# Kernel optimization log

Hardware: AMD Instinct MI355X
Metric: run time of the kernel (lower is better)

The kernel has to match this reference:

```python
import jax, jax.numpy as jnp
import numpy as np

B, DIM, IN_DIM, H, W = 4, 256, 128, 128, 128
DD = IN_DIM // 2          # down_dim = 64
HEADS = 8
BN_EPS = 1e-5


def conv2d(x, w, b=None, pad=0, dil=1):
    y = jax.lax.conv_general_dilated(
        x, w, window_strides=(1, 1),
        padding=[(pad, pad), (pad, pad)],
        rhs_dilation=(dil, dil),
        dimension_numbers=('NCHW', 'OIHW', 'NCHW'))
    if b is not None:
        y = y + b[None, :, None, None]
    return y


def bn_relu(x, s, o):
    # eval-mode BatchNorm2d with running_mean=0, running_var=1
    return jax.nn.relu(x * (s / np.sqrt(1.0 + BN_EPS))[None, :, None, None] + o[None, :, None, None])


def setup_inputs() -> dict:
    ks = iter(jax.random.split(jax.random.key(0), 80))

    def w(shape, sc=0.05):
        return sc * jax.random.normal(next(ks), shape, jnp.float32)

    def s(c):
        return 1.0 + 0.1 * jax.random.normal(next(ks), (c,), jnp.float32)

    def o(c):
        return 0.02 * jax.random.normal(next(ks), (c,), jnp.float32)

    d = {}
    d['x'] = jax.random.normal(next(ks), (B, DIM, H, W), jnp.float32)
    d['w_dc'] = w((IN_DIM, DIM, 3, 3)); d['b_dc'] = w((IN_DIM,)); d['s_dc'] = s(IN_DIM); d['o_dc'] = o(IN_DIM)
    d['w1'] = w((DD, IN_DIM, 1, 1)); d['b1'] = w((DD,)); d['s1'] = s(DD); d['o1'] = o(DD)
    d['w2'] = w((DD, DD, 3, 3)); d['b2'] = w((DD,)); d['s2'] = s(DD); d['o2'] = o(DD)
    d['w3'] = w((DD, DD, 3, 3)); d['b3'] = w((DD,)); d['s3'] = s(DD); d['o3'] = o(DD)
    d['w4'] = w((DD, DD, 3, 3)); d['b4'] = w((DD,)); d['s4'] = s(DD); d['o4'] = o(DD)
    d['w5'] = w((DD, IN_DIM, 1, 1)); d['b5'] = w((DD,)); d['s5'] = s(DD); d['o5'] = o(DD)
    d['temperature'] = jnp.ones((HEADS, 1, 1), jnp.float32)
    d['w_po'] = w((DD, 2 * DD, 1, 1))  # project_out, bias=False
    d['w_wa'] = w((DD // 16, DD, 1, 1)); d['b_wa'] = w((DD // 16,)); d['s_wa'] = s(DD // 16); d['o_wa'] = o(DD // 16)
    d['w_wb'] = w((DD, DD // 16, 1, 1)); d['b_wb'] = w((DD,))
    d['w_f'] = w((DD, 5 * DD, 1, 1)); d['b_f'] = w((DD,)); d['s_f'] = s(DD); d['o_f'] = o(DD)
    d['w_oa'] = w((DD // 2, DD, 3, 3)); d['b_oa'] = w((DD // 2,)); d['s_oa'] = s(DD // 2); d['o_oa'] = o(DD // 2)
    d['w_ob'] = w((1, DD // 2, 1, 1)); d['b_ob'] = w((1,))
    return d


def reference(x, w_dc, b_dc, s_dc, o_dc, w1, b1, s1, o1, w2, b2, s2, o2,
              w3, b3, s3, o3, w4, b4, s4, o4, w5, b5, s5, o5,
              temperature, w_po, w_wa, b_wa, s_wa, o_wa, w_wb, b_wb,
              w_f, b_f, s_f, o_f, w_oa, b_oa, s_oa, o_oa, w_ob, b_ob):

    def branch(c):
        b, ch, h, wd = c.shape
        f = jnp.fft.fft2(c)                                   # [b,ch,h,w] complex64 (q=k=v=tepqkv)
        qkv = f.reshape(b, HEADS, ch // HEADS, h * wd)        # v (unnormalized)
        n = jnp.sqrt(jnp.sum(jnp.square(jnp.abs(qkv)), axis=-1, keepdims=True))
        qn = qkv / jnp.maximum(n, 1e-12)                      # F.normalize(dim=-1); q == k
        attn = jnp.einsum('bhcn,bhdn->bhcd', qn, qn) * temperature
        # custom complex normalization: separate real/imag softmax
        attn = jax.lax.complex(jax.nn.softmax(attn.real, axis=-1),
                               jax.nn.softmax(attn.imag, axis=-1))
        of = jnp.abs(jnp.fft.ifft2(jnp.einsum('bhcd,bhdn->bhcn', attn, qkv)))  # ifft2 over (c, hw)
        of = of.reshape(b, ch, h, wd)
        g = jax.nn.sigmoid(conv2d(bn_relu(conv2d(f.real, w_wa, b_wa), s_wa, o_wa), w_wb, b_wb))
        ol = jnp.abs(jnp.fft.ifft2(g * f))                    # ifft2 over (h, w)
        return conv2d(jnp.concatenate([of, ol], axis=1), w_po) + c

    xd = bn_relu(conv2d(x, w_dc, b_dc, pad=1), s_dc, o_dc)
    c1 = bn_relu(conv2d(xd, w1, b1), s1, o1)
    c2 = bn_relu(conv2d(c1, w2, b2, pad=3, dil=3), s2, o2)
    F2 = branch(c2)
    c3 = bn_relu(conv2d(c1 + F2, w3, b3, pad=5, dil=5), s3, o3)
    F3 = branch(c3)
    c4 = bn_relu(conv2d(c1 + F3, w4, b4, pad=7, dil=7), s4, o4)
    F4 = branch(c4)
    # conv5: global avg pool -> 1x1 conv -> bilinear upsample of a 1x1 map == broadcast
    c5 = bn_relu(conv2d(jnp.mean(xd, axis=(2, 3), keepdims=True), w5, b5), s5, o5)
    c5 = jnp.broadcast_to(c5, (c5.shape[0], c5.shape[1], xd.shape[2], xd.shape[3]))
    fused = bn_relu(conv2d(jnp.concatenate([c1, F2, F3, F4, c5], axis=1), w_f, b_f), s_f, o_f)
    return conv2d(bn_relu(conv2d(fused, w_oa, b_oa, pad=1), s_oa, o_oa), w_ob, b_ob)
```

## Files before the change

### kernel.cpp

```cpp
#include <hip/hip_runtime.h>

#define S 16384
#define PI_F 3.14159265358979f

struct Ptrs { const float* p[43]; };

enum : int {
  O_SBDC=0, O_SB1=256, O_SB2=512, O_SB3=768, O_SB4=1024, O_SB5=1280,
  O_SBWA=1536, O_SBF=1792, O_SBOA=2048,
  O_M=2304, O_C5=2816, O_NRM=3072, O_GRAM=3328, O_ATT2=7424, O_BEFF=11520,
  O_WB=16384,
  O_PART=147456,
  O_H=180224,
  O_WP=442368,
  O_A=524288,
  O_FIN=8912896,
  O_CC=25690112,
  O_DRE=29884416, O_DIMG=34078720,
  O_ERE=38273024, O_EIM=42467328,
  O_G=46661632
};

typedef short bfrag __attribute__((ext_vector_type(8)));
typedef float ffrag __attribute__((ext_vector_type(4)));

__device__ __forceinline__ float bf2f(unsigned short u){
  union { unsigned int i; float f; } v; v.i = ((unsigned int)u) << 16; return v.f;
}
__device__ __forceinline__ unsigned short f2bf(float f){
  unsigned int x = __float_as_uint(f);
  unsigned int r = x + 0x7fffu + ((x >> 16) & 1u);
  return (unsigned short)(r >> 16);
}

__global__ void prep_sb_kernel(Ptrs P, float* ws){
  const float r = rsqrtf(1.0f + 1e-5f);
  int bi=0, si=0, oi=0, C=0, dst=0;
  switch (blockIdx.x){
    case 0: bi=2; si=3; oi=4; C=128; dst=O_SBDC; break;
    case 1: bi=6; si=7; oi=8; C=64; dst=O_SB1; break;
    case 2: bi=10; si=11; oi=12; C=64; dst=O_SB2; break;
    case 3: bi=14; si=15; oi=16; C=64; dst=O_SB3; break;
    case 4: bi=18; si=19; oi=20; C=64; dst=O_SB4; break;
    case 5: bi=22; si=23; oi=24; C=64; dst=O_SB5; break;
    case 6: bi=28; si=29; oi=30; C=4;  dst=O_SBWA; break;
    case 7: bi=34; si=35; oi=36; C=64; dst=O_SBF; break;
    default: bi=38; si=39; oi=40; C=32; dst=O_SBOA; break;
  }
  for (int c = threadIdx.x; c < C; c += 256){
    float bb = P.p[bi][c], ss = P.p[si][c], oo = P.p[oi][c];
    float sc = ss * r;
    ws[dst + c] = sc;
    ws[dst + C + c] = bb * sc + oo;
  }
}

__global__ __launch_bounds__(256) void xpad_kernel(const float* __restrict__ x,
    unsigned short* __restrict__ XT){
  int yy = blockIdx.x, b = blockIdx.y;
  long obase = ((long)(b*130) + yy) * (130L*256);
  int tid = threadIdx.x;
  if (yy == 0 || yy == 129){
    uint4 z; z.x=0; z.y=0; z.z=0; z.w=0;
    for (int i = tid; i < 130*256/8; i += 256)
      *(uint4*)(XT + obase + (long)i*8) = z;
    return;
  }
  __shared__ float LT[64][129];
  int y = yy - 1;
  for (int c0 = 0; c0 < 256; c0 += 64){
    for (int idx = tid; idx < 64*128; idx += 256){
      int ci = idx >> 7, xx = idx & 127;
      LT[ci][xx] = x[((long)(b*256 + c0 + ci)*128 + y)*128 + xx];
    }
    __syncthreads();
    for (int idx = tid; idx < 128*16; idx += 256){
      int xp = idx >> 4, c4 = (idx & 15)*4;
      ushort4 v;
      v.x = f2bf(LT[c4][xp]);   v.y = f2bf(LT[c4+1][xp]);
      v.z = f2bf(LT[c4+2][xp]); v.w = f2bf(LT[c4+3][xp]);
      *(ushort4*)(XT + obase + (long)(xp+1)*256 + c0 + c4) = v;
    }
    __syncthreads();
  }
  if (tid < 64){
    ushort4 z; z.x=0; z.y=0; z.z=0; z.w=0;
    *(ushort4*)(XT + obase + tid*4) = z;
    *(ushort4*)(XT + obase + 129L*256 + tid*4) = z;
  }
}

__global__ void wt_kernel(const float* __restrict__ w, unsigned short* __restrict__ WH,
    unsigned short* __restrict__ WL){
  for (int e = blockIdx.x*256 + threadIdx.x; e < 294912; e += gridDim.x*256){
    int c32 = e & 31, co = (e >> 5) & 127, kc = (e >> 12) & 7, sh = e >> 15;
    int ky = sh / 3, kx = sh - ky*3;
    int ci = kc*32 + c32;
    float v = w[((long)(co*256 + ci)*3 + ky)*3 + kx];
    unsigned short h = f2bf(v);
    WH[e] = h;
    WL[e] = f2bf(v - bf2f(h));
  }
}

__global__ void wtg_kernel(Ptrs P, unsigned short* __restrict__ WB){
  const float* w; int cout; long off;
  switch (blockIdx.y){
    case 0: w = P.p[9];  cout = 64; off = 0;      break;
    case 1: w = P.p[13]; cout = 64; off = 73728;  break;
    case 2: w = P.p[17]; cout = 64; off = 147456; break;
    default: w = P.p[37]; cout = 32; off = 221184; break;
  }
  int total = 576*cout;
  unsigned short* WH = WB + off;
  unsigned short* WL = WH + total;
  for (int e = blockIdx.x*256 + threadIdx.x; e < total; e += gridDim.x*256){
    int c32 = e & 31;
    int co = (e >> 5) & (cout - 1);
    int kc = (e / (32*cout)) & 1;
    int sh = e / (64*cout);
    int ky = sh/3, kx = sh - ky*3;
    int ci = kc*32 + c32;
    float v = w[((long)(co*64 + ci)*3 + ky)*3 + kx];
    unsigned short h = f2bf(v);
    WH[e] = h;
    WL[e] = f2bf(v - bf2f(h));
  }
}

__global__ void wtp_kernel(Ptrs P, unsigned short* __restrict__ WP){
  const float* w; int KC, wstr; long off;
  switch (blockIdx.y){
    case 0: w = P.p[5];  KC = 4; wstr = 128; off = 0;     break;
    case 1: w = P.p[26]; KC = 4; wstr = 128; off = 16384; break;
    default: w = P.p[33]; KC = 8; wstr = 320; off = 32768; break;
  }
  int total = KC*64*32;
  unsigned short* WH = WP + off;
  unsigned short* WL = WH + total;
  for (int e = blockIdx.x*256 + threadIdx.x; e < total; e += gridDim.x*256){
    int c32 = e & 31, co = (e >> 5) & 63, kc = e >> 11;
    float v = w[(long)co*wstr + kc*32 + c32];
    unsigned short h = f2bf(v);
    WH[e] = h;
    WL[e] = f2bf(v - bf2f(h));
  }
}

template<int DIL>
__global__ __launch_bounds__(256) void xpad64_kernel(const float* __restrict__ in1,
    const float* __restrict__ in2, long in_bs, unsigned short* __restrict__ XP){
  constexpr int TW = 128 + 2*DIL;
  int yy = blockIdx.x, b = blockIdx.y;
  long obase = (long)(b*TW + yy) * TW * 64;
  int tid = threadIdx.x;
  if (yy < DIL || yy >= 128 + DIL){
    uint4 z; z.x=0; z.y=0; z.z=0; z.w=0;
    for (int i = tid; i < TW*8; i += 256)
      *(uint4*)(XP + obase + (long)i*8) = z;
    return;
  }
  __shared__ float LT[64][129];
  int y = yy - DIL;
  const float* p1 = in1 + (long)b*in_bs + (long)y*128;
  const float* p2 = in2 ? in2 + (long)b*in_bs + (long)y*128 : nullptr;
  for (int idx = tid; idx < 64*128; idx += 256){
    int ci = idx >> 7, xx = idx & 127;
    float v = p1[(long)ci*S + xx];
    if (p2) v += p2[(long)ci*S + xx];
    LT[ci][xx] = v;
  }
  __syncthreads();
  for (int i = tid; i < 2*DIL*16; i += 256){
    int side = i / (DIL*16);
    int r = i - side*(DIL*16);
    int xcol = side ? (128 + DIL + (r >> 4)) : (r >> 4);
    ushort4 z; z.x=0; z.y=0; z.z=0; z.w=0;
    *(ushort4*)(XP + obase + (long)xcol*64 + (r & 15)*4) = z;
  }
  for (int idx = tid; idx < 128*16; idx += 256){
    int xp = idx >> 4, c4 = (idx & 15)*4;
    ushort4 v;
    v.x = f2bf(LT[c4][xp]);   v.y = f2bf(LT[c4+1][xp]);
    v.z = f2bf(LT[c4+2][xp]); v.w = f2bf(LT[c4+3][xp]);
    *(ushort4*)(XP + obase + (long)(xp + DIL)*64 + c4) = v;
  }
}

template<int DIL, int KC, int NBLK>
__global__ __launch_bounds__(256) void conv3x3_mfma_kernel(
    const unsigned short* __restrict__ XP,
    const unsigned short* __restrict__ WH, const unsigned short* __restrict__ WL,
    const float* __restrict__ scbi, float* __restrict__ out){
  constexpr int CIN = KC*32;
  constexpr int TW = 128 + 2*DIL;
  constexpr int STEPS = 9*KC;
  constexpr int MI = (NBLK == 64) ? 4 : 2;
  constexpr int LDA = 36;
  __shared__ unsigned short Als[128*LDA];
  __shared__ unsigned short BHs[NBLK*LDA];
  __shared__ unsigned short BLs[NBLK*LDA];
  int bid = blockIdx.x;
  int y = (bid & 7)*16 + ((bid >> 3) & 15);
  int b = (bid >> 7) & 3;
  int n2 = bid >> 9;
  int nb = gridDim.x >> 9; if (nb == 0) nb = 1;
  int coutTotal = nb * NBLK;
  int tid = threadIdx.x, wv = tid >> 6, lane = tid & 63;
  int mt0 = (NBLK == 64) ? (wv & 1)*4 : wv*2;
  int nt0 = (NBLK == 64) ? (wv >> 1)*2 : 0;
  ffrag acc[MI][2];
  #pragma unroll
  for (int i = 0; i < MI; i++)
    #pragma unroll
    for (int j = 0; j < 2; j++)
      #pragma unroll
      for (int r = 0; r < 4; r++) acc[i][j][r] = 0.f;

  int pixq = tid >> 2, qq = tid & 3;
  int kq = (lane >> 4)*8, rown = lane & 15;
  int wrA0 = pixq*LDA + qq*8;
  int wrA1 = (pixq + 64)*LDA + qq*8;
  int wrB  = (tid >> 2)*LDA + qq*8;

  uint4 A0, A1, BHr, BLr;
  {
    long abase = ((long)(b*TW + y)*TW)*CIN + qq*8;
    A0 = *(const uint4*)(XP + abase + (long)pixq*CIN);
    A1 = *(const uint4*)(XP + abase + (long)(pixq + 64)*CIN);
    long gw = (long)n2*NBLK*32;
    if (NBLK == 64 || tid < 128){
      BHr = *(const uint4*)(WH + gw + tid*8);
      BLr = *(const uint4*)(WL + gw + tid*8);
    }
  }
  for (int step = 0; step < STEPS; step++){
    __syncthreads();
    *(uint4*)&Als[wrA0] = A0;
    *(uint4*)&Als[wrA1] = A1;
    if (NBLK == 64 || tid < 128){
      *(uint4*)&BHs[wrB] = BHr;
      *(uint4*)&BLs[wrB] = BLr;
    }
    __syncthreads();
    if (step + 1 < STEPS){
      int s2 = step + 1;
      int sh = s2 / KC, kc = s2 - sh*KC;
      int ky = sh / 3, kx = sh - ky*3;
      long abase = ((long)(b*TW + y + ky*DIL)*TW + kx*DIL)*CIN + kc*32 + qq*8;
      A0 = *(const uint4*)(XP + abase + (long)pixq*CIN);
      A1 = *(const uint4*)(XP + abase + (long)(pixq + 64)*CIN);
      long gw = ((long)s2*coutTotal + n2*NBLK)*32;
      if (NBLK == 64 || tid < 128){
        BHr = *(const uint4*)(WH + gw + tid*8);
        BLr = *(const uint4*)(WL + gw + tid*8);
      }
    }
    bfrag af[MI], bhf[2], blf[2];
    #pragma unroll
    for (int i = 0; i < MI; i++)
      af[i] = *(const bfrag*)&Als[((mt0 + i)*16 + rown)*LDA + kq];
    #pragma unroll
    for (int j = 0; j < 2; j++){
      bhf[j] = *(const bfrag*)&BHs[((nt0 + j)*16 + rown)*LDA + kq];
      blf[j] = *(const bfrag*)&BLs[((nt0 + j)*16 + rown)*LDA + kq];
    }
    #pragma unroll
    for (int i = 0; i < MI; i++)
      #pragma unroll
      for (int j = 0; j < 2; j++){
        acc[i][j] = __builtin_amdgcn_mfma_f32_16x16x32_bf16(af[i], blf[j], acc[i][j], 0, 0, 0);
        acc[i][j] = __builtin_amdgcn_mfma_f32_16x16x32_bf16(af[i], bhf[j], acc[i][j], 0, 0, 0);
      }
  }
  #pragma unroll
  for (int i = 0; i < MI; i++){
    int pixel = (mt0 + i)*16 + (lane >> 4)*4;
    #pragma unroll
    for (int j = 0; j < 2; j++){
      int co = n2*NBLK + (nt0 + j)*16 + (lane & 15);
      float sc = scbi[co], bb = scbi[coutTotal + co];
      float* op = out + ((long)(b*coutTotal + co))*S + y*128 + pixel;
      #pragma unroll
      for (int r = 0; r < 4; r++)
        op[r] = fmaxf(acc[i][j][r]*sc + bb, 0.f);
    }
  }
}

template<int MODE, int KC, int BF16IN>
__global__ __launch_bounds__(256) void conv1x1_mfma_kernel(
    const void* __restrict__ inv, long in_bs,
    const unsigned short* __restrict__ WH, const unsigned short* __restrict__ WL,
    const float* __restrict__ scbi, const float* __restrict__ beff,
    const float* __restrict__ res, long res_bs,
    float* __restrict__ out, long out_bs){
  constexpr int LDA = 36;
  __shared__ unsigned short Als[128*LDA];
  __shared__ unsigned short BHs[64*LDA];
  __shared__ unsigned short BLs[64*LDA];
  int bid = blockIdx.x;
  int y = (bid & 7)*16 + ((bid >> 3) & 15);
  int b = bid >> 7;
  int tid = threadIdx.x, wv = tid >> 6, lane = tid & 63;
  int mt0 = (wv & 1)*4, nt0 = (wv >> 1)*2;
  ffrag acc[4][2];
  #pragma unroll
  for (int i = 0; i < 4; i++)
    #pragma unroll
    for (int j = 0; j < 2; j++)
      #pragma unroll
      for (int r = 0; r < 4; r++) acc[i][j][r] = 0.f;
  int pq = tid & 31, cg = tid >> 5;
  int kq = (lane >> 4)*8, rown = lane & 15;
  int wrB = (tid >> 2)*LDA + (tid & 3)*8;
  const float* ibf = (const float*)inv + (long)b*in_bs + y*128;
  const unsigned short* ibs = (const unsigned short*)inv + (long)b*in_bs + y*128;
  unsigned short a[16];
  uint4 BHr, BLr;
  #pragma unroll
  for (int cc = 0; cc < 4; cc++)
    #pragma unroll
    for (int i = 0; i < 4; i++){
      if (BF16IN) a[cc*4 + i] = ibs[(long)(cg*4 + cc)*S + pq + 32*i];
      else        a[cc*4 + i] = f2bf(ibf[(long)(cg*4 + cc)*S + pq + 32*i]);
    }
  BHr = *(const uint4*)(WH + tid*8);
  BLr = *(const uint4*)(WL + tid*8);
  for (int kc = 0; kc < KC; kc++){
    __syncthreads();
    #pragma unroll
    for (int i = 0; i < 4; i++){
      ushort4 v;
      v.x = a[0 + i];  v.y = a[4 + i];
      v.z = a[8 + i];  v.w = a[12 + i];
      *(ushort4*)&Als[(pq + 32*i)*LDA + cg*4] = v;
    }
    *(uint4*)&BHs[wrB] = BHr;
    *(uint4*)&BLs[wrB] = BLr;
    __syncthreads();
    if (kc + 1 < KC){
      #pragma unroll
      for (int cc = 0; cc < 4; cc++)
        #pragma unroll
        for (int i = 0; i < 4; i++){
          long off = (long)((kc + 1)*32 + cg*4 + cc)*S + pq + 32*i;
          if (BF16IN) a[cc*4 + i] = ibs[off];
          else        a[cc*4 + i] = f2bf(ibf[off]);
        }
      long gw = (long)(kc + 1)*2048;
      BHr = *(const uint4*)(WH + gw + tid*8);
      BLr = *(const uint4*)(WL + gw + tid*8);
    }
    bfrag af[4], bhf[2], blf[2];
    #pragma unroll
    for (int i = 0; i < 4; i++)
      af[i] = *(const bfrag*)&Als[((mt0 + i)*16 + rown)*LDA + kq];
    #pragma unroll
    for (int j = 0; j < 2; j++){
      bhf[j] = *(const bfrag*)&BHs[((nt0 + j)*16 + rown)*LDA + kq];
      blf[j] = *(const bfrag*)&BLs[((nt0 + j)*16 + rown)*LDA + kq];
    }
    #pragma unroll
    for (int i = 0; i < 4; i++)
      #pragma unroll
      for (int j = 0; j < 2; j++){
        acc[i][j] = __builtin_amdgcn_mfma_f32_16x16x32_bf16(af[i], blf[j], acc[i][j], 0, 0, 0);
        acc[i][j] = __builtin_amdgcn_mfma_f32_16x16x32_bf16(af[i], bhf[j], acc[i][j], 0, 0, 0);
      }
  }
  #pragma unroll
  for (int i = 0; i < 4; i++){
    int pixel = (mt0 + i)*16 + (lane >> 4)*4;
    #pragma unroll
    for (int j = 0; j < 2; j++){
      int co = (nt0 + j)*16 + (lane & 15);
      float* op = out + (long)b*out_bs + (long)co*S + y*128 + pixel;
      #pragma unroll
      for (int r = 0; r < 4; r++){
        float v = acc[i][j][r];
        if (MODE == 0){
          v = fmaxf(v*scbi[co] + scbi[64 + co], 0.f);
        } else if (MODE == 1){
          v += res[(long)b*res_bs + (long)co*S + y*128 + pixel + r];
        } else {
          v = fmaxf(v*scbi[co] + beff[b*64 + co], 0.f);
        }
        op[r] = v;
      }
    }
  }
}

__device__ __forceinline__ void fft128_mk_tw(float (&tws)[8], float (&twc)[8],
                                             float sign, int lane){
  float a0 = sign * (2.0f*PI_F/128.0f) * (float)lane;
  __sincosf(a0, &tws[0], &twc[0]);
  int i = 1;
  #pragma unroll
  for (int h = 32; h >= 1; h >>= 1, i++){
    int j = lane & (h - 1);
    float a = sign * (2.0f*PI_F/128.0f) * (float)(j * (64/h));
    __sincosf(a, &tws[i], &twc[i]);
  }
}

__device__ __forceinline__ void fft128(float& z0r, float& z0i, float& z1r, float& z1i,
    const float (&tws)[8], const float (&twc)[8], int lane){
  {
    float ar = z0r, ai = z0i, br = z1r, bi = z1i;
    z0r = ar + br; z0i = ai + bi;
    float dr = ar - br, di = ai - bi;
    float s = tws[0], c = twc[0];
    z1r = dr*c - di*s; z1i = dr*s + di*c;
  }
  int idx = 1;
  #pragma unroll
  for (int h = 32; h >= 1; h >>= 1, idx++){
    float s = tws[idx], c = twc[idx];
    bool up = (lane & h) != 0;
    float pr, pi, nr, ni;
    pr = __shfl_xor(z0r, h, 64); pi = __shfl_xor(z0i, h, 64);
    if (!up){ nr = z0r + pr; ni = z0i + pi; }
    else { float dr = pr - z0r, di = pi - z0i; nr = dr*c - di*s; ni = dr*s + di*c; }
    z0r = nr; z0i = ni;
    pr = __shfl_xor(z1r, h, 64); pi = __shfl_xor(z1i, h, 64);
    if (!up){ nr = z1r + pr; ni = z1i + pi; }
    else { float dr = pr - z1r, di = pi - z1i; nr = dr*c - di*s; ni = dr*s + di*c; }
    z1r = nr; z1i = ni;
  }
}

__global__ __launch_bounds__(256) void fft_rows_fwd_kernel(const float* __restrict__ in,
    unsigned short* __restrict__ outRe, unsigned short* __restrict__ outIm){
  int line = blockIdx.x*4 + (threadIdx.x >> 6);
  int lane = threadIdx.x & 63;
  float tws[8], twc[8];
  fft128_mk_tw(tws, twc, -1.0f, lane);
  long ib = (long)line * 128;
  float z0r = in[ib + lane], z0i = 0.f;
  float z1r = in[ib + lane + 64], z1i = 0.f;
  fft128(z0r, z0i, z1r, z1i, tws, twc, lane);
  int k = __brev(lane) >> 25;
  ushort2 vr; vr.x = f2bf(z0r); vr.y = f2bf(z1r);
  ushort2 vi; vi.x = f2bf(z0i); vi.y = f2bf(z1i);
  *(ushort2*)(outRe + ib + k) = vr;
  *(ushort2*)(outIm + ib + k) = vi;
}

template<int MODE>
__global__ __launch_bounds__(256) void fft_cols_kernel(
    const unsigned short* inRe, const unsigned short* inIm,
    unsigned short* outRe, unsigned short* outIm,
    const float* gate, const float* wb, const float* bwb){
  __shared__ float lre[128][17];
  __shared__ float lim[128][17];
  int plane = blockIdx.y;
  int cb = blockIdx.x * 16;
  int tid = threadIdx.x;
  long pbase = (long)plane * S;
  float w0=0.f, w1=0.f, w2=0.f, w3=0.f, bw=0.f;
  const float* Hb = nullptr;
  if (MODE == 1){
    int co = plane & 63;
    w0 = wb[co*4]; w1 = wb[co*4+1]; w2 = wb[co*4+2]; w3 = wb[co*4+3];
    bw = bwb[co];
    Hb = gate + (long)(plane >> 6) * 4 * S;
  }
  #pragma unroll
  for (int i = 0; i < 8; i++){
    int idx = tid + i*256;
    int r = idx >> 4, c = idx & 15;
    int pxl = r*128 + cb + c;
    long a = pbase + pxl;
    float re = bf2f(inRe[a]), im = bf2f(inIm[a]);
    if (MODE == 1){
      float hv = bw + w0*Hb[pxl] + w1*Hb[S + pxl] + w2*Hb[2*S + pxl] + w3*Hb[3*S + pxl];
      float g = 1.0f / (1.0f + __expf(-hv));
      re *= g; im *= g;
    }
    lre[r][c] = re; lim[r][c] = im;
  }
  __syncthreads();
  int wv = tid >> 6, lane = tid & 63;
  const float sign = (MODE == 0) ? -1.0f : 1.0f;
  float tws[8], twc[8];
  fft128_mk_tw(tws, twc, sign, lane);
  #pragma unroll
  for (int cc = 0; cc < 4; cc++){
    int c = wv*4 + cc;
    float z0r = lre[lane][c], z0i = lim[lane][c];
    float z1r = lre[lane + 64][c], z1i = lim[lane + 64][c];
    fft128(z0r, z0i, z1r, z1i, tws, twc, lane);
    int k = __brev(lane) >> 25;
    if (MODE == 2){
      int n2 = cb + c;
      float s, co;
      float a0 = (2.0f*PI_F/16384.0f) * (float)(n2 * k);
      __sincosf(a0, &s, &co);
      float t = z0r*co - z0i*s; z0i = z0r*s + z0i*co; z0r = t;
      float a1 = (2.0f*PI_F/16384.0f) * (float)(n2 * (k + 1));
      __sincosf(a1, &s, &co);
      t = z1r*co - z1i*s; z1i = z1r*s + z1i*co; z1r = t;
    }
    lre[k][c] = z0r;     lim[k][c] = z0i;
    lre[k + 1][c] = z1r; lim[k + 1][c] = z1i;
  }
  __syncthreads();
  #pragma unroll
  for (int i = 0; i < 8; i++){
    int idx = tid + i*256;
    int r = idx >> 4, c = idx & 15;
    long a = pbase + r*128 + cb + c;
    outRe[a] = f2bf(lre[r][c]); outIm[a] = f2bf(lim[r][c]);
  }
}

__global__ __launch_bounds__(256) void ifft_rows_abs_ol_kernel(
    const unsigned short* __restrict__ Ere, const unsigned short* __restrict__ Eim,
    unsigned short* __restrict__ AB){
  int line = blockIdx.x*4 + (threadIdx.x >> 6);
  int lane = threadIdx.x & 63;
  float tws[8], twc[8];
  fft128_mk_tw(tws, twc, 1.0f, lane);
  int plane = line >> 7, row = line & 127;
  long ib = (long)plane*S + row*128;
  float z0r = bf2f(Ere[ib + lane]), z0i = bf2f(Eim[ib + lane]);
  float z1r = bf2f(Ere[ib + lane + 64]), z1i = bf2f(Eim[ib + lane + 64]);
  fft128(z0r, z0i, z1r, z1i, tws, twc, lane);
  int b = plane >> 6, ch = plane & 63;
  unsigned short* out = AB + ((long)(b*128 + 64 + ch)) * S + row*128;
  int k = __brev(lane) >> 25;
  ushort2 v;
  v.x = f2bf(sqrtf(z0r*z0r + z0i*z0i) * (1.0f/16384.0f));
  v.y = f2bf(sqrtf(z1r*z1r + z1i*z1i) * (1.0f/16384.0f));
  *(ushort2*)(out + k) = v;
}

__global__ __launch_bounds__(256) void ifft_rows_abs_ofT_kernel(
    const unsigned short* __restrict__ Ere, const unsigned short* __restrict__ Eim,
    unsigned short* __restrict__ AB){
  __shared__ float T[128][17];
  int plane = blockIdx.y;
  int r0 = blockIdx.x * 16;
  int wv = threadIdx.x >> 6, lane = threadIdx.x & 63;
  float tws[8], twc[8];
  fft128_mk_tw(tws, twc, 1.0f, lane);
  #pragma unroll
  for (int i = 0; i < 4; i++){
    int rl = wv*4 + i;
    int row = r0 + rl;
    long ib = (long)plane*S + row*128;
    float z0r = bf2f(Ere[ib + lane]), z0i = bf2f(Eim[ib + lane]);
    float z1r = bf2f(Ere[ib + lane + 64]), z1i = bf2f(Eim[ib + lane + 64]);
    fft128(z0r, z0i, z1r, z1i, tws, twc, lane);
    int k = __brev(lane) >> 25;
    T[k][rl]     = sqrtf(z0r*z0r + z0i*z0i) * (1.0f/16384.0f);
    T[k + 1][rl] = sqrtf(z1r*z1r + z1i*z1i) * (1.0f/16384.0f);
  }
  __syncthreads();
  int b = plane >> 6, ch = plane & 63;
  unsigned short* out = AB + ((long)(b*128 + ch)) * S + r0;
  #pragma unroll
  for (int i = 0; i < 8; i++){
    int idx = threadIdx.x + i*256;
    int k2 = idx >> 4, rl = idx & 15;
    out[(long)k2*128 + rl] = f2bf(T[k2][rl]);
  }
}

__global__ __launch_bounds__(256) void gram_part_kernel(
    const unsigned short* __restrict__ Dre, const unsigned short* __restrict__ Dim,
    float* __restrict__ PART){
  int bh = blockIdx.x, slab = blockIdx.y;
  long base = (long)bh * 8 * S;
  int n0 = slab * 2048;
  float accr[36], acci[36], nsq[8];
  #pragma unroll
  for (int i = 0; i < 36; i++){ accr[i] = 0.f; acci[i] = 0.f; }
  #pragma unroll
  for (int i = 0; i < 8; i++) nsq[i] = 0.f;
  for (int it = 0; it < 8; it++){
    int n = n0 + it*256 + threadIdx.x;
    float xr[8], xi[8];
    #pragma unroll
    for (int c = 0; c < 8; c++){
      xr[c] = bf2f(Dre[base + (long)c*S + n]);
      xi[c] = bf2f(Dim[base + (long)c*S + n]);
      nsq[c] += xr[c]*xr[c] + xi[c]*xi[c];
    }
    int t = 0;
    #pragma unroll
    for (int c = 0; c < 8; c++)
      #pragma unroll
      for (int d = c; d < 8; d++){
        accr[t] += xr[c]*xr[d] - xi[c]*xi[d];
        acci[t] += xr[c]*xi[d] + xi[c]*xr[d];
        t++;
      }
  }
  __shared__ float red[4][80];
  int wv = threadIdx.x >> 6, lane = threadIdx.x & 63;
  #pragma unroll
  for (int i = 0; i < 80; i++){
    float v = (i < 36) ? accr[i] : (i < 72) ? acci[i - 36] : nsq[i - 72];
    #pragma unroll
    for (int o = 32; o; o >>= 1) v += __shfl_xor(v, o, 64);
    if (lane == 0) red[wv][i] = v;
  }
  __syncthreads();
  if (threadIdx.x < 80){
    int i = threadIdx.x;
    PART[(long)(bh*8 + slab)*80 + i] = red[0][i] + red[1][i] + red[2][i] + red[3][i];
  }
}

__global__ void attn2f_kernel(const float* __restrict__ PART,
    const float* __restrict__ temp, float* __restrict__ ATT2){
  __shared__ float ssum[80];
  __shared__ float sar[64], sai[64];
  int bh = blockIdx.x;
  int t = threadIdx.x;
  if (t < 80){
    float s = 0.f;
    for (int i = 0; i < 8; i++) s += PART[(long)(bh*8 + i)*80 + t];
    ssum[t] = s;
  }
  __syncthreads();
  if (t >= 64) return;
  int lane = t;
  int c = lane >> 3, d = lane & 7;
  int lo = min(c, d), hi = max(c, d);
  int t2 = lo*8 - lo*(lo - 1)/2 + (hi - lo);
  float nnc = fmaxf(sqrtf(ssum[72 + c]), 1e-12f);
  float nnd = fmaxf(sqrtf(ssum[72 + d]), 1e-12f);
  float inv = temp[bh & 7] / (nnc * nnd);
  float ar = ssum[t2] * inv, ai = ssum[36 + t2] * inv;
  float m = ar;
  m = fmaxf(m, __shfl_xor(m, 1, 64)); m = fmaxf(m, __shfl_xor(m, 2, 64)); m = fmaxf(m, __shfl_xor(m, 4, 64));
  float e = __expf(ar - m);
  float su = e;
  su += __shfl_xor(su, 1, 64); su += __shfl_xor(su, 2, 64); su += __shfl_xor(su, 4, 64);
  ar = e / su;
  m = ai;
  m = fmaxf(m, __shfl_xor(m, 1, 64)); m = fmaxf(m, __shfl_xor(m, 2, 64)); m = fmaxf(m, __shfl_xor(m, 4, 64));
  e = __expf(ai - m);
  su = e;
  su += __shfl_xor(su, 1, 64); su += __shfl_xor(su, 2, 64); su += __shfl_xor(su, 4, 64);
  ai = e / su;
  sar[lane] = ar; sai[lane] = ai;
  __syncthreads();
  const float ct[8] = {1.f, 0.70710678f, 0.f, -0.70710678f, -1.f, -0.70710678f, 0.f, 0.70710678f};
  const float st[8] = {0.f, 0.70710678f, 1.f, 0.70710678f, 0.f, -0.70710678f, -1.f, -0.70710678f};
  int cp = c;
  float sr = 0.f, si = 0.f;
  #pragma unroll
  for (int cc = 0; cc < 8; cc++){
    int k = (cc * cp) & 7;
    float a = sar[cc*8 + d], b2 = sai[cc*8 + d];
    sr += ct[k]*a - st[k]*b2;
    si += ct[k]*b2 + st[k]*a;
  }
  float2 v; v.x = sr * 0.125f; v.y = si * 0.125f;
  ((float2*)ATT2)[bh*64 + lane] = v;
}

__global__ __launch_bounds__(256) void apply_attn_kernel(
    const unsigned short* __restrict__ Dre, const unsigned short* __restrict__ Dim,
    const float* __restrict__ ATT2,
    unsigned short* __restrict__ Ere, unsigned short* __restrict__ Eim){
  int bh = blockIdx.y;
  int px = blockIdx.x*1024 + (threadIdx.x & 63)*4 + (threadIdx.x >> 6)*256;
  long base = (long)bh * 8 * S + px;
  float4 ar[8], ai[8];
  #pragma unroll
  for (int i = 0; i < 8; i++){
    ar[i].x = ar[i].y = ar[i].z = ar[i].w = 0.f;
    ai[i].x = ai[i].y = ai[i].z = ai[i].w = 0.f;
  }
  #pragma unroll
  for (int d = 0; d < 8; d++){
    ushort4 ur = *(const ushort4*)(Dre + base + (long)d*S);
    ushort4 ui = *(const ushort4*)(Dim + base + (long)d*S);
    float4 xr, xi;
    xr.x = bf2f(ur.x); xr.y = bf2f(ur.y); xr.z = bf2f(ur.z); xr.w = bf2f(ur.w);
    xi.x = bf2f(ui.x); xi.y = bf2f(ui.y); xi.z = bf2f(ui.z); xi.w = bf2f(ui.w);
    #pragma unroll
    for (int cp = 0; cp < 8; cp++){
      float wr = ATT2[bh*128 + (cp*8 + d)*2];
      float wi = ATT2[bh*128 + (cp*8 + d)*2 + 1];
      ar[cp].x += wr*xr.x - wi*xi.x;  ai[cp].x += wr*xi.x + wi*xr.x;
      ar[cp].y += wr*xr.y - wi*xi.y;  ai[cp].y += wr*xi.y + wi*xr.y;
      ar[cp].z += wr*xr.z - wi*xi.z;  ai[cp].z += wr*xi.z + wi*xr.z;
      ar[cp].w += wr*xr.w - wi*xi.w;  ai[cp].w += wr*xi.w + wi*xr.w;
    }
  }
  #pragma unroll
  for (int cp = 0; cp < 8; cp++){
    ushort4 vr, vi;
    vr.x = f2bf(ar[cp].x); vr.y = f2bf(ar[cp].y); vr.z = f2bf(ar[cp].z); vr.w = f2bf(ar[cp].w);
    vi.x = f2bf(ai[cp].x); vi.y = f2bf(ai[cp].y); vi.z = f2bf(ai[cp].z); vi.w = f2bf(ai[cp].w);
    *(ushort4*)(Ere + base + (long)cp*S) = vr;
    *(ushort4*)(Eim + base + (long)cp*S) = vi;
  }
}

__global__ __launch_bounds__(256) void gateh_kernel(const unsigned short* __restrict__ Dre,
    const float* __restrict__ wa, const float* __restrict__ sbwa, float* __restrict__ H){
  int b = blockIdx.y;
  int px = blockIdx.x*256 + threadIdx.x;
  long base = (long)b * 64 * S + px;
  float h0 = 0.f, h1 = 0.f, h2 = 0.f, h3 = 0.f;
  for (int ci = 0; ci < 64; ci++){
    float x = bf2f(Dre[base + (long)ci*S]);
    h0 += wa[ci]*x; h1 += wa[64 + ci]*x; h2 += wa[128 + ci]*x; h3 += wa[192 + ci]*x;
  }
  long ob = (long)b * 4 * S + px;
  H[ob]       = fmaxf(h0*sbwa[0] + sbwa[4], 0.f);
  H[ob + S]   = fmaxf(h1*sbwa[1] + sbwa[5], 0.f);
  H[ob + 2*S] = fmaxf(h2*sbwa[2] + sbwa[6], 0.f);
  H[ob + 3*S] = fmaxf(h3*sbwa[3] + sbwa[7], 0.f);
}

__global__ __launch_bounds__(256) void mean_kernel(const float* __restrict__ A, float* __restrict__ M){
  int p = blockIdx.x;
  long base = (long)p * S;
  float s = 0.f;
  for (int n = threadIdx.x; n < S; n += 256) s += A[base + n];
  #pragma unroll
  for (int o = 32; o; o >>= 1) s += __shfl_xor(s, o, 64);
  __shared__ float sm[4];
  if ((threadIdx.x & 63) == 0) sm[threadIdx.x >> 6] = s;
  __syncthreads();
  if (threadIdx.x == 0) M[p] = (sm[0] + sm[1] + sm[2] + sm[3]) * (1.0f/16384.0f);
}

__global__ void c5_kernel(const float* __restrict__ W5, const float* __restrict__ sb5,
    const float* __restrict__ M, float* __restrict__ C5){
  int t = threadIdx.x;
  if (t >= 256) return;
  int b = t >> 6, co = t & 63;
  float s = 0.f;
  for (int ci = 0; ci < 128; ci++) s += W5[co*128 + ci] * M[b*128 + ci];
  C5[t] = fmaxf(s * sb5[co] + sb5[64 + co], 0.f);
}

__global__ void beff_kernel(const float* __restrict__ WF, const float* __restrict__ sbf,
    const float* __restrict__ C5, float* __restrict__ BEFF){
  int t = threadIdx.x;
  if (t >= 256) return;
  int b = t >> 6, co = t & 63;
  float s = 0.f;
  for (int j = 0; j < 64; j++) s += WF[co*320 + 256 + j] * C5[b*64 + j];
  BEFF[t] = s * sbf[co] + sbf[64 + co];
}

__global__ __launch_bounds__(256) void ob_kernel(const float* __restrict__ Tin,
    const float* __restrict__ wob, const float* __restrict__ bob, float* __restrict__ out){
  int b = blockIdx.y;
  int px = blockIdx.x*1024 + (threadIdx.x & 63)*4 + (threadIdx.x >> 6)*256;
  float b0 = bob[0];
  float4 a; a.x = b0; a.y = b0; a.z = b0; a.w = b0;
  for (int ci = 0; ci < 32; ci++){
    float4 v = *(const float4*)(Tin + ((long)b*32 + ci)*S + px);
    float w = wob[ci];
    a.x += w*v.x; a.y += w*v.y; a.z += w*v.z; a.w += w*v.w;
  }
  *(float4*)(out + (long)b*S + px) = a;
}

extern "C" void kernel_launch(void* const* d_in, const int* in_sizes, int n_in,
                              void* d_out, int out_size, void* d_ws, size_t ws_size,
                              hipStream_t stream){
  float* ws = (float*)d_ws;
  Ptrs P;
  for (int i = 0; i < 43 && i < n_in; i++) P.p[i] = (const float*)d_in[i];
  float* out = (float*)d_out;

  float* A   = ws + O_A;
  float* FIN = ws + O_FIN;
  float* CC  = ws + O_CC;
  float* G   = ws + O_G;
  float* H   = ws + O_H;

  unsigned short* DRE16 = (unsigned short*)(ws + O_DRE);
  unsigned short* DIM16 = (unsigned short*)(ws + O_DIMG);
  unsigned short* ERE16 = (unsigned short*)(ws + O_ERE);
  unsigned short* EIM16 = (unsigned short*)(ws + O_EIM);
  unsigned short* AB    = (unsigned short*)(ws + O_A);

  unsigned short* XT  = (unsigned short*)(ws + O_DRE);
  unsigned short* WHd = (unsigned short*)(ws + O_CC);
  unsigned short* WLd = (unsigned short*)(ws + O_CC + 147456);
  unsigned short* WB  = (unsigned short*)(ws + O_WB);
  unsigned short* WP  = (unsigned short*)(ws + O_WP);
  unsigned short* XP  = (unsigned short*)(ws + O_ERE);

  prep_sb_kernel<<<dim3(9), dim3(256), 0, stream>>>(P, ws);
  xpad_kernel<<<dim3(130, 4), dim3(256), 0, stream>>>(P.p[0], XT);
  wt_kernel<<<dim3(128), dim3(256), 0, stream>>>(P.p[1], WHd, WLd);
  wtg_kernel<<<dim3(16, 4), dim3(256), 0, stream>>>(P, WB);
  wtp_kernel<<<dim3(8, 3), dim3(256), 0, stream>>>(P, WP);

  conv3x3_mfma_kernel<1,8,64><<<dim3(1024), dim3(256), 0, stream>>>(
      XT, WHd, WLd, ws + O_SBDC, A);

  mean_kernel<<<dim3(512), dim3(256), 0, stream>>>(A, ws + O_M);
  c5_kernel<<<dim3(1), dim3(256), 0, stream>>>(P.p[21], ws + O_SB5, ws + O_M, ws + O_C5);
  beff_kernel<<<dim3(1), dim3(256), 0, stream>>>(P.p[33], ws + O_SBF, ws + O_C5, ws + O_BEFF);

  conv1x1_mfma_kernel<0,4,0><<<dim3(512), dim3(256), 0, stream>>>(
      A, 128*S, WP, WP + 8192, ws + O_SB1, nullptr, nullptr, 0, FIN, 256*S);

  for (int k = 0; k < 3; k++){
    const float* sb = ws + (k == 0 ? O_SB2 : k == 1 ? O_SB3 : O_SB4);
    const float* in2 = (k == 0) ? nullptr : FIN + (long)(64*k)*S;
    unsigned short* wh = WB + (k == 0 ? 0 : k == 1 ? 73728 : 147456);
    if (k == 0){
      xpad64_kernel<3><<<dim3(134, 4), dim3(256), 0, stream>>>(FIN, in2, 256*S, XP);
      conv3x3_mfma_kernel<3,2,64><<<dim3(512), dim3(256), 0, stream>>>(
          XP, wh, wh + 36864, sb, CC);
    } else if (k == 1){
      xpad64_kernel<5><<<dim3(138, 4), dim3(256), 0, stream>>>(FIN, in2, 256*S, XP);
      conv3x3_mfma_kernel<5,2,64><<<dim3(512), dim3(256), 0, stream>>>(
          XP, wh, wh + 36864, sb, CC);
    } else {
      xpad64_kernel<7><<<dim3(142, 4), dim3(256), 0, stream>>>(FIN, in2, 256*S, XP);
      conv3x3_mfma_kernel<7,2,64><<<dim3(512), dim3(256), 0, stream>>>(
          XP, wh, wh + 36864, sb, CC);
    }

    fft_rows_fwd_kernel<<<dim3(8192), dim3(256), 0, stream>>>(CC, DRE16, DIM16);
    fft_cols_kernel<0><<<dim3(8, 256), dim3(256), 0, stream>>>(
        DRE16, DIM16, DRE16, DIM16, nullptr, nullptr, nullptr);
    gram_part_kernel<<<dim3(32, 8), dim3(256), 0, stream>>>(DRE16, DIM16, ws + O_PART);
    attn2f_kernel<<<dim3(32), dim3(128), 0, stream>>>(ws + O_PART, P.p[25], ws + O_ATT2);
    gateh_kernel<<<dim3(64, 4), dim3(256), 0, stream>>>(DRE16, P.p[27], ws + O_SBWA, H);
    fft_cols_kernel<1><<<dim3(8, 256), dim3(256), 0, stream>>>(
        DRE16, DIM16, ERE16, EIM16, H, P.p[31], P.p[32]);
    ifft_rows_abs_ol_kernel<<<dim3(8192), dim3(256), 0, stream>>>(ERE16, EIM16, AB);
    apply_attn_kernel<<<dim3(16, 32), dim3(256), 0, stream>>>(DRE16, DIM16, ws + O_ATT2, ERE16, EIM16);
    fft_cols_kernel<2><<<dim3(8, 256), dim3(256), 0, stream>>>(
        ERE16, EIM16, ERE16, EIM16, nullptr, nullptr, nullptr);
    ifft_rows_abs_ofT_kernel<<<dim3(8, 256), dim3(256), 0, stream>>>(ERE16, EIM16, AB);
    conv1x1_mfma_kernel<1,4,1><<<dim3(512), dim3(256), 0, stream>>>(
        AB, 128*S, WP + 16384, WP + 24576, nullptr, nullptr, CC, 64*S,
        FIN + (long)(64*(k + 1))*S, 256*S);
  }

  conv1x1_mfma_kernel<2,8,0><<<dim3(512), dim3(256), 0, stream>>>(
      FIN, 256*S, WP + 32768, WP + 49152, ws + O_SBF, ws + O_BEFF, nullptr, 0, CC, 64*S);
  xpad64_kernel<1><<<dim3(130, 4), dim3(256), 0, stream>>>(CC, nullptr, 64*S, XP);
  conv3x3_mfma_kernel<1,2,32><<<dim3(512), dim3(256), 0, stream>>>(
      XP, WB + 221184, WB + 221184 + 18432, ws + O_SBOA, G);
  ob_kernel<<<dim3(16, 4), dim3(256), 0, stream>>>(G, P.p[41], P.p[42], out);
}
```

Before: 984.2 us.

## Fuse row and column FFT passes into whole-plane 2D FFT kernels in LDS

Replaces the separate row-FFT and column-FFT kernels (three pairs per branch) with single kernels that each hold a whole 128x128 complex plane in shared memory and do both passes with 1024 threads per block. This drops the bf16 intermediate round trips through global memory and cuts the number of launches. The cost is about 132KB of LDS per block, so only one block fits per CU, and each grid has just 256 blocks, which lowers occupancy and latency hiding. It also keeps intermediates in fp32 rather than bf16 between the two passes.

After: 909.4 us. 1.08x faster.

```diff
diff --git a/kernel.cpp b/kernel.cpp
--- a/kernel.cpp
+++ b/kernel.cpp
@@ -431,141 +431,163 @@
   }
 }
 
-__global__ __launch_bounds__(256) void fft_rows_fwd_kernel(const float* __restrict__ in,
+
+__global__ __launch_bounds__(1024) void fft2_fwd_kernel(const float* __restrict__ in,
     unsigned short* __restrict__ outRe, unsigned short* __restrict__ outIm){
-  int line = blockIdx.x*4 + (threadIdx.x >> 6);
-  int lane = threadIdx.x & 63;
+  __shared__ float lre[128][129];
+  __shared__ float lim[128][129];
+  int plane = blockIdx.x;
+  int tid = threadIdx.x, wv = tid >> 6, lane = tid & 63;
+  long pbase = (long)plane * S;
+  for (int i = tid; i < S/4; i += 1024){
+    int px = i*4; int r = px >> 7, c = px & 127;
+    float4 v = *(const float4*)(in + pbase + px);
+    lre[r][c] = v.x; lre[r][c+1] = v.y; lre[r][c+2] = v.z; lre[r][c+3] = v.w;
+  }
   float tws[8], twc[8];
   fft128_mk_tw(tws, twc, -1.0f, lane);
-  long ib = (long)line * 128;
-  float z0r = in[ib + lane], z0i = 0.f;
-  float z1r = in[ib + lane + 64], z1i = 0.f;
-  fft128(z0r, z0i, z1r, z1i, tws, twc, lane);
-  int k = __brev(lane) >> 25;
-  ushort2 vr; vr.x = f2bf(z0r); vr.y = f2bf(z1r);
-  ushort2 vi; vi.x = f2bf(z0i); vi.y = f2bf(z1i);
-  *(ushort2*)(outRe + ib + k) = vr;
-  *(ushort2*)(outIm + ib + k) = vi;
-}
-
-template<int MODE>
-__global__ __launch_bounds__(256) void fft_cols_kernel(
-    const unsigned short* inRe, const unsigned short* inIm,
-    unsigned short* outRe, unsigned short* outIm,
-    const float* gate, const float* wb, const float* bwb){
-  __shared__ float lre[128][17];
-  __shared__ float lim[128][17];
-  int plane = blockIdx.y;
-  int cb = blockIdx.x * 16;
-  int tid = threadIdx.x;
-  long pbase = (long)plane * S;
-  float w0=0.f, w1=0.f, w2=0.f, w3=0.f, bw=0.f;
-  const float* Hb = nullptr;
-  if (MODE == 1){
-    int co = plane & 63;
-    w0 = wb[co*4]; w1 = wb[co*4+1]; w2 = wb[co*4+2]; w3 = wb[co*4+3];
-    bw = bwb[co];
-    Hb = gate + (long)(plane >> 6) * 4 * S;
-  }
-  #pragma unroll
-  for (int i = 0; i < 8; i++){
-    int idx = tid + i*256;
-    int r = idx >> 4, c = idx & 15;
-    int pxl = r*128 + cb + c;
-    long a = pbase + pxl;
-    float re = bf2f(inRe[a]), im = bf2f(inIm[a]);
-    if (MODE == 1){
-      float hv = bw + w0*Hb[pxl] + w1*Hb[S + pxl] + w2*Hb[2*S + pxl] + w3*Hb[3*S + pxl];
-      float g = 1.0f / (1.0f + __expf(-hv));
-      re *= g; im *= g;
-    }
-    lre[r][c] = re; lim[r][c] = im;
-  }
-  __syncthreads();
-  int wv = tid >> 6, lane = tid & 63;
-  const float sign = (MODE == 0) ? -1.0f : 1.0f;
-  float tws[8], twc[8];
-  fft128_mk_tw(tws, twc, sign, lane);
-  #pragma unroll
-  for (int cc = 0; cc < 4; cc++){
-    int c = wv*4 + cc;
+  __syncthreads();
+  #pragma unroll
+  for (int rr = 0; rr < 8; rr++){
+    int r = wv*8 + rr;
+    float z0r = lre[r][lane], z0i = 0.f;
+    float z1r = lre[r][lane + 64], z1i = 0.f;
+    fft128(z0r, z0i, z1r, z1i, tws, twc, lane);
+    int k = __brev(lane) >> 25;
+    lre[r][k] = z0r;     lim[r][k] = z0i;
+    lre[r][k+1] = z1r;   lim[r][k+1] = z1i;
+  }
+  __syncthreads();
+  #pragma unroll
+  for (int cc = 0; cc < 8; cc++){
+    int c = wv*8 + cc;
     float z0r = lre[lane][c], z0i = lim[lane][c];
     float z1r = lre[lane + 64][c], z1i = lim[lane + 64][c];
     fft128(z0r, z0i, z1r, z1i, tws, twc, lane);
     int k = __brev(lane) >> 25;
-    if (MODE == 2){
-      int n2 = cb + c;
-      float s, co;
-      float a0 = (2.0f*PI_F/16384.0f) * (float)(n2 * k);
-      __sincosf(a0, &s, &co);
-      float t = z0r*co - z0i*s; z0i = z0r*s + z0i*co; z0r = t;
-      float a1 = (2.0f*PI_F/16384.0f) * (float)(n2 * (k + 1));
-      __sincosf(a1, &s, &co);
-      t = z1r*co - z1i*s; z1i = z1r*s + z1i*co; z1r = t;
-    }
     lre[k][c] = z0r;     lim[k][c] = z0i;
-    lre[k + 1][c] = z1r; lim[k + 1][c] = z1i;
-  }
-  __syncthreads();
-  #pragma unroll
-  for (int i = 0; i < 8; i++){
-    int idx = tid + i*256;
-    int r = idx >> 4, c = idx & 15;
-    long a = pbase + r*128 + cb + c;
-    outRe[a] = f2bf(lre[r][c]); outIm[a] = f2bf(lim[r][c]);
-  }
-}
-
-__global__ __launch_bounds__(256) void ifft_rows_abs_ol_kernel(
+    lre[k+1][c] = z1r;   lim[k+1][c] = z1i;
+  }
+  __syncthreads();
+  for (int i = tid; i < S/2; i += 1024){
+    int px = i*2; int r = px >> 7, c = px & 127;
+    ushort2 vr, vi;
+    vr.x = f2bf(lre[r][c]); vr.y = f2bf(lre[r][c+1]);
+    vi.x = f2bf(lim[r][c]); vi.y = f2bf(lim[r][c+1]);
+    *(ushort2*)(outRe + pbase + px) = vr;
+    *(ushort2*)(outIm + pbase + px) = vi;
+  }
+}
+
+__global__ __launch_bounds__(1024) void ifft2_gate_abs_ol_kernel(
+    const unsigned short* __restrict__ Dre, const unsigned short* __restrict__ Dim,
+    const float* __restrict__ H, const float* __restrict__ wb, const float* __restrict__ bwb,
+    unsigned short* __restrict__ AB){
+  __shared__ float lre[128][129];
+  __shared__ float lim[128][129];
+  int plane = blockIdx.x;
+  int b = plane >> 6, ch = plane & 63;
+  int tid = threadIdx.x, wv = tid >> 6, lane = tid & 63;
+  long pbase = (long)plane * S;
+  float w0 = wb[ch*4], w1 = wb[ch*4+1], w2 = wb[ch*4+2], w3 = wb[ch*4+3];
+  float bw = bwb[ch];
+  const float* Hb = H + (long)b*4*S;
+  for (int i = tid; i < S; i += 1024){
+    int r = i >> 7, c = i & 127;
+    float hv = bw + w0*Hb[i] + w1*Hb[S + i] + w2*Hb[2*S + i] + w3*Hb[3*S + i];
+    float g = 1.0f / (1.0f + __expf(-hv));
+    lre[r][c] = bf2f(Dre[pbase + i]) * g;
+    lim[r][c] = bf2f(Dim[pbase + i]) * g;
+  }
+  float tws[8], twc[8];
+  fft128_mk_tw(tws, twc, 1.0f, lane);
+  __syncthreads();
+  #pragma unroll
+  for (int cc = 0; cc < 8; cc++){
+    int c = wv*8 + cc;
+    float z0r = lre[lane][c], z0i = lim[lane][c];
+    float z1r = lre[lane + 64][c], z1i = lim[lane + 64][c];
+    fft128(z0r, z0i, z1r, z1i, tws, twc, lane);
+    int k = __brev(lane) >> 25;
+    lre[k][c] = z0r;     lim[k][c] = z0i;
+    lre[k+1][c] = z1r;   lim[k+1][c] = z1i;
+  }
+  __syncthreads();
+  unsigned short* out = AB + ((long)(b*128 + 64 + ch)) * S;
+  #pragma unroll
+  for (int rr = 0; rr < 8; rr++){
+    int r = wv*8 + rr;
+    float z0r = lre[r][lane], z0i = lim[r][lane];
+    float z1r = lre[r][lane + 64], z1i = lim[r][lane + 64];
+    fft128(z0r, z0i, z1r, z1i, tws, twc, lane);
+    int k = __brev(lane) >> 25;
+    ushort2 v;
+    v.x = f2bf(sqrtf(z0r*z0r + z0i*z0i) * (1.0f/16384.0f));
+    v.y = f2bf(sqrtf(z1r*z1r + z1i*z1i) * (1.0f/16384.0f));
+    *(ushort2*)(out + (long)r*128 + k) = v;
+  }
+}
+
+__global__ __launch_bounds__(1024) void ifft2_abs_ofT_kernel(
     const unsigned short* __restrict__ Ere, const unsigned short* __restrict__ Eim,
     unsigned short* __restrict__ AB){
-  int line = blockIdx.x*4 + (threadIdx.x >> 6);
-  int lane = threadIdx.x & 63;
+  __shared__ float lre[128][129];
+  __shared__ float lim[128][129];
+  int plane = blockIdx.x;
+  int b = plane >> 6, ch = plane & 63;
+  int tid = threadIdx.x, wv = tid >> 6, lane = tid & 63;
+  long pbase = (long)plane * S;
+  for (int i = tid; i < S; i += 1024){
+    int r = i >> 7, c = i & 127;
+    lre[r][c] = bf2f(Ere[pbase + i]);
+    lim[r][c] = bf2f(Eim[pbase + i]);
+  }
   float tws[8], twc[8];
   fft128_mk_tw(tws, twc, 1.0f, lane);
-  int plane = line >> 7, row = line & 127;
-  long ib = (long)plane*S + row*128;
-  float z0r = bf2f(Ere[ib + lane]), z0i = bf2f(Eim[ib + lane]);
-  float z1r = bf2f(Ere[ib + lane + 64]), z1i = bf2f(Eim[ib + lane + 64]);
-  fft128(z0r, z0i, z1r, z1i, tws, twc, lane);
-  int b = plane >> 6, ch = plane & 63;
-  unsigned short* out = AB + ((long)(b*128 + 64 + ch)) * S + row*128;
-  int k = __brev(lane) >> 25;
-  ushort2 v;
-  v.x = f2bf(sqrtf(z0r*z0r + z0i*z0i) * (1.0f/16384.0f));
-  v.y = f2bf(sqrtf(z1r*z1r + z1i*z1i) * (1.0f/16384.0f));
-  *(ushort2*)(out + k) = v;
-}
-
-__global__ __launch_bounds__(256) void ifft_rows_abs_ofT_kernel(
-    const unsigned short* __restrict__ Ere, const unsigned short* __restrict__ Eim,
-    unsigned short* __restrict__ AB){
-  __shared__ float T[128][17];
-  int plane = blockIdx.y;
-  int r0 = blockIdx.x * 16;
-  int wv = threadIdx.x >> 6, lane = threadIdx.x & 63;
-  float tws[8], twc[8];
-  fft128_mk_tw(tws, twc, 1.0f, lane);
-  #pragma unroll
-  for (int i = 0; i < 4; i++){
-    int rl = wv*4 + i;
-    int row = r0 + rl;
-    long ib = (long)plane*S + row*128;
-    float z0r = bf2f(Ere[ib + lane]), z0i = bf2f(Eim[ib + lane]);
-    float z1r = bf2f(Ere[ib + lane + 64]), z1i = bf2f(Eim[ib + lane + 64]);
+  __syncthreads();
+  #pragma unroll
+  for (int cc = 0; cc < 8; cc++){
+    int c = wv*8 + cc;
+    float z0r = lre[lane][c], z0i = lim[lane][c];
+    float z1r = lre[lane + 64][c], z1i = lim[lane + 64][c];
     fft128(z0r, z0i, z1r, z1i, tws, twc, lane);
     int k = __brev(lane) >> 25;
-    T[k][rl]     = sqrtf(z0r*z0r + z0i*z0i) * (1.0f/16384.0f);
-    T[k + 1][rl] = sqrtf(z1r*z1r + z1i*z1i) * (1.0f/16384.0f);
-  }
-  __syncthreads();
-  int b = plane >> 6, ch = plane & 63;
-  unsigned short* out = AB + ((long)(b*128 + ch)) * S + r0;
-  #pragma unroll
-  for (int i = 0; i < 8; i++){
-    int idx = threadIdx.x + i*256;
-    int k2 = idx >> 4, rl = idx & 15;
-    out[(long)k2*128 + rl] = f2bf(T[k2][rl]);
+    float s, co;
+    float a0 = (2.0f*PI_F/16384.0f) * (float)(c * k);
+    __sincosf(a0, &s, &co);
+    float t = z0r*co - z0i*s; z0i = z0r*s + z0i*co; z0r = t;
+    float a1 = (2.0f*PI_F/16384.0f) * (float)(c * (k + 1));
+    __sincosf(a1, &s, &co);
+    t = z1r*co - z1i*s; z1i = z1r*s + z1i*co; z1r = t;
+    lre[k][c] = z0r;     lim[k][c] = z0i;
+    lre[k+1][c] = z1r;   lim[k+1][c] = z1i;
+  }
+  __syncthreads();
+  float absv[8][2];
+  #pragma unroll
+  for (int rr = 0; rr < 8; rr++){
+    int r = wv*8 + rr;
+    float z0r = lre[r][lane], z0i = lim[r][lane];
+    float z1r = lre[r][lane + 64], z1i = lim[r][lane + 64];
+    fft128(z0r, z0i, z1r, z1i, tws, twc, lane);
+    absv[rr][0] = sqrtf(z0r*z0r + z0i*z0i) * (1.0f/16384.0f);
+    absv[rr][1] = sqrtf(z1r*z1r + z1i*z1i) * (1.0f/16384.0f);
+  }
+  __syncthreads();
+  int k2 = __brev(lane) >> 25;
+  #pragma unroll
+  for (int rr = 0; rr < 8; rr++){
+    int r = wv*8 + rr;
+    lre[k2][r] = absv[rr][0];
+    lre[k2+1][r] = absv[rr][1];
+  }
+  __syncthreads();
+  unsigned short* out = AB + ((long)(b*128 + ch)) * S;
+  for (int i = tid; i < S/2; i += 1024){
+    int px = i*2; int r = px >> 7, c = px & 127;
+    ushort2 v;
+    v.x = f2bf(lre[r][c]); v.y = f2bf(lre[r][c+1]);
+    *(ushort2*)(out + px) = v;
   }
 }
 
@@ -830,19 +852,14 @@
           XP, wh, wh + 36864, sb, CC);
     }
 
-    fft_rows_fwd_kernel<<<dim3(8192), dim3(256), 0, stream>>>(CC, DRE16, DIM16);
-    fft_cols_kernel<0><<<dim3(8, 256), dim3(256), 0, stream>>>(
-        DRE16, DIM16, DRE16, DIM16, nullptr, nullptr, nullptr);
+    fft2_fwd_kernel<<<dim3(256), dim3(1024), 0, stream>>>(CC, DRE16, DIM16);
     gram_part_kernel<<<dim3(32, 8), dim3(256), 0, stream>>>(DRE16, DIM16, ws + O_PART);
     attn2f_kernel<<<dim3(32), dim3(128), 0, stream>>>(ws + O_PART, P.p[25], ws + O_ATT2);
     gateh_kernel<<<dim3(64, 4), dim3(256), 0, stream>>>(DRE16, P.p[27], ws + O_SBWA, H);
-    fft_cols_kernel<1><<<dim3(8, 256), dim3(256), 0, stream>>>(
-        DRE16, DIM16, ERE16, EIM16, H, P.p[31], P.p[32]);
-    ifft_rows_abs_ol_kernel<<<dim3(8192), dim3(256), 0, stream>>>(ERE16, EIM16, AB);
+    ifft2_gate_abs_ol_kernel<<<dim3(256), dim3(1024), 0, stream>>>(
+        DRE16, DIM16, H, P.p[31], P.p[32], AB);
     apply_attn_kernel<<<dim3(16, 32), dim3(256), 0, stream>>>(DRE16, DIM16, ws + O_ATT2, ERE16, EIM16);
-    fft_cols_kernel<2><<<dim3(8, 256), dim3(256), 0, stream>>>(
-        ERE16, EIM16, ERE16, EIM16, nullptr, nullptr, nullptr);
-    ifft_rows_abs_ofT_kernel<<<dim3(8, 256), dim3(256), 0, stream>>>(ERE16, EIM16, AB);
+    ifft2_abs_ofT_kernel<<<dim3(256), dim3(1024), 0, stream>>>(ERE16, EIM16, AB);
     conv1x1_mfma_kernel<1,4,1><<<dim3(512), dim3(256), 0, stream>>>(
         AB, 128*S, WP + 16384, WP + 24576, nullptr, nullptr, CC, 64*S,
         FIN + (long)(64*(k + 1))*S, 256*S);
```
